# Performance work log

Hardware: AMD Instinct MI355X
Metric: run time of the kernel (lower is better)

Reference implementation:

```python
import jax, jax.numpy as jnp
import numpy as np

N = 100000
E = 1600000
DIN = 165
DH = 128


def setup_inputs() -> dict:
    key = jax.random.key(0)
    ks = jax.random.split(key, 10)
    def nrm(k, shape, scale=0.1):
        return jax.random.normal(k, shape, dtype=jnp.float32) * scale
    x = jax.random.normal(ks[0], (N, DIN), dtype=jnp.float32)
    edge_index = jax.random.randint(ks[1], (2, E), 0, N, dtype=jnp.int64)
    return dict(
        x=x,
        edge_index=edge_index,
        fb_w1=nrm(ks[2], (DIN, DIN // 2)),
        fb_w2=nrm(ks[3], (DIN // 2, DIN)),
        sage_wl=nrm(ks[4], (DIN, DH)),
        sage_bl=jnp.zeros((DH,), jnp.float32),
        sage_wr=nrm(ks[5], (DIN, DH)),
        gat_w=nrm(ks[6], (DH, DH // 2)),
        gat_att_src=nrm(ks[7], (DH // 2,)),
        gat_att_dst=nrm(ks[8], (DH // 2,)),
        gat_b=jnp.zeros((DH // 2,), jnp.float32),
        cheb_w=nrm(ks[9], (DH // 2, 1)),
        cheb_b=jnp.zeros((1,), jnp.float32),
    )


def _segment_softmax(logits, seg, num_segments):
    mx = jax.ops.segment_max(logits, seg, num_segments=num_segments)
    e = jnp.exp(logits - mx[seg])
    s = jax.ops.segment_sum(e, seg, num_segments=num_segments)
    return e / (s[seg] + 1e-16)


def reference(x, edge_index, fb_w1, fb_w2, sage_wl, sage_bl, sage_wr,
              gat_w, gat_att_src, gat_att_dst, gat_b, cheb_w, cheb_b):
    n = x.shape[0]
    src, dst = edge_index[0], edge_index[1]

    # FeatureBooster: scatter over batch=arange(n) is identity for max and sum,
    # so max_result == sum_result == x and y = sigmoid(mlp(x) + mlp(x)).
    m = jnp.maximum(x @ fb_w1, 0.0) @ fb_w2
    x = x * jax.nn.sigmoid(m + m)

    # SAGEConv (mean aggregation): out = lin_l(mean_agg(x_src -> dst)) + lin_r(x)
    agg = jax.ops.segment_sum(x[src], dst, num_segments=n)  # [n, DIN]
    cnt = jax.ops.segment_sum(jnp.ones((src.shape[0],), x.dtype), dst, num_segments=n)
    agg = agg / jnp.maximum(cnt, 1.0)[:, None]
    x = agg @ sage_wl + sage_bl + x @ sage_wr
    x = jnp.maximum(x, 0.0)  # relu; dropout is identity in eval mode

    # GATConv (heads=1) with default add_self_loops=True
    ar = jnp.arange(n, dtype=src.dtype)
    si = jnp.concatenate([src, ar])
    di = jnp.concatenate([dst, ar])
    h = x @ gat_w                      # [n, 64]
    a_s = h @ gat_att_src              # [n]
    a_d = h @ gat_att_dst              # [n]
    e = a_s[si] + a_d[di]
    e = jnp.where(e > 0, e, 0.2 * e)   # leaky_relu slope 0.2
    alpha = _segment_softmax(e, di, n)
    x = jax.ops.segment_sum(h[si] * alpha[:, None], di, num_segments=n) + gat_b
    x = jnp.maximum(x, 0.0)

    # ChebConv with K=1: T_0(x) = x, so it's a plain linear layer.
    x = x @ cheb_w + cheb_b
    return jax.nn.sigmoid(x)
```

## Files before the change

### kernel.cpp

```cpp
#include <hip/hip_runtime.h>
#include <hip/hip_bf16.h>

#define N_NODES 100000
#define N_EDGES 1600000
#define DIN 165
#define DHID 82
#define DH 128
#define DG 64

typedef _Float16 f16;
typedef f16 f16x8 __attribute__((ext_vector_type(8)));
typedef f16 f16x4 __attribute__((ext_vector_type(4)));
typedef f16 f16x2 __attribute__((ext_vector_type(2)));
typedef float f32x4 __attribute__((ext_vector_type(4)));

#define MFMA16(a, b, c) __builtin_amdgcn_mfma_f32_16x16x32_f16(a, b, c, 0, 0, 0)


__global__ __launch_bounds__(256) void xpad_kernel(const float* __restrict__ x,
                                                   f16* __restrict__ Xp) {
    int gid = blockIdx.x * 256 + threadIdx.x;
    int node = gid / 48, g = gid % 48;
    int col0 = g * 4;
    f16x4 o;
#pragma unroll
    for (int j = 0; j < 4; j++) {
        int c = col0 + j;
        o[j] = (f16)((c < DIN) ? x[(long)node * DIN + c] : 0.f);
    }
    *((f16x4*)(Xp + (long)node * 192 + col0)) = o;
}

__global__ __launch_bounds__(256) void h_kernel(const f16* __restrict__ Xp,
                                                const float* __restrict__ w1,
                                                f16* __restrict__ H) {
    int tid = threadIdx.x, wave = tid >> 6, lane = tid & 63;
    int q = lane >> 4, l16 = lane & 15;
    int blk = blockIdx.x;
    int g = (blk >> 3) & 1;
    int chunk = (blk & 7) + 8 * (blk >> 4);
    int nbase = g * 48;
    f16x8 bf[3][6];
#pragma unroll
    for (int nt = 0; nt < 3; nt++) {
        int col = nbase + nt * 16 + l16;
#pragma unroll
        for (int ks = 0; ks < 6; ks++) {
            int kb = ks * 32 + q * 8;
            f16x8 b;
#pragma unroll
            for (int j = 0; j < 8; j++) {
                int k = kb + j;
                b[j] = (f16)((k < DIN && col < DHID) ? w1[k * DHID + col] : 0.f);
            }
            bf[nt][ks] = b;
        }
    }
    for (int mt = chunk * 4 + wave; mt < 6250; mt += 768) {
        const f16* xr = Xp + (long)(mt * 16 + l16) * 192;
        f32x4 acc[3];
#pragma unroll
        for (int nt = 0; nt < 3; nt++) acc[nt] = (f32x4){0.f, 0.f, 0.f, 0.f};
#pragma unroll
        for (int ks = 0; ks < 6; ks++) {
            f16x8 a = *((const f16x8*)(xr + ks * 32 + q * 8));
#pragma unroll
            for (int nt = 0; nt < 3; nt++) acc[nt] = MFMA16(a, bf[nt][ks], acc[nt]);
        }
#pragma unroll
        for (int nt = 0; nt < 3; nt++) {
            int col = nbase + nt * 16 + l16;
#pragma unroll
            for (int r = 0; r < 4; r++) {
                int node = mt * 16 + q * 4 + r;
                H[(long)node * 96 + col] = (f16)fmaxf(acc[nt][r], 0.f);
            }
        }
    }
}

__global__ __launch_bounds__(256) void y_kernel(const f16* __restrict__ Xp,
                                                const f16* __restrict__ H,
                                                const float* __restrict__ w2,
                                                f16* __restrict__ Y) {
    int tid = threadIdx.x, wave = tid >> 6, lane = tid & 63;
    int q = lane >> 4, l16 = lane & 15;
    int blk = blockIdx.x;
    int g = (blk >> 3) & 3;
    int chunk = (blk & 7) + 8 * (blk >> 5);
    int nbase = g * 48;
    f16x8 bf[3][3];
#pragma unroll
    for (int nt = 0; nt < 3; nt++) {
        int col = nbase + nt * 16 + l16;
#pragma unroll
        for (int ks = 0; ks < 3; ks++) {
            int kb = ks * 32 + q * 8;
            f16x8 b;
#pragma unroll
            for (int j = 0; j < 8; j++) {
                int k = kb + j;
                b[j] = (f16)((k < DHID && col < DIN) ? w2[k * DIN + col] : 0.f);
            }
            bf[nt][ks] = b;
        }
    }
    for (int mt = chunk * 4 + wave; mt < 6250; mt += 768) {
        const f16* hr = H + (long)(mt * 16 + l16) * 96;
        f32x4 acc[3];
#pragma unroll
        for (int nt = 0; nt < 3; nt++) acc[nt] = (f32x4){0.f, 0.f, 0.f, 0.f};
#pragma unroll
        for (int ks = 0; ks < 3; ks++) {
            f16x8 a = *((const f16x8*)(hr + ks * 32 + q * 8));
#pragma unroll
            for (int nt = 0; nt < 3; nt++) acc[nt] = MFMA16(a, bf[nt][ks], acc[nt]);
        }
#pragma unroll
        for (int nt = 0; nt < 3; nt++) {
            int col = nbase + nt * 16 + l16;
#pragma unroll
            for (int r = 0; r < 4; r++) {
                int node = mt * 16 + q * 4 + r;
                float gg = 1.f / (1.f + __expf(-2.f * acc[nt][r]));
                float xv = (float)Xp[(long)node * 192 + col];
                Y[(long)node * 192 + col] = (f16)(xv * gg);
            }
        }
    }
}

__global__ __launch_bounds__(256) void sage_lin_kernel(const f16* __restrict__ Y,
                                                       const float* __restrict__ wl,
                                                       const float* __restrict__ wr,
                                                       const float* __restrict__ bl,
                                                       f16* __restrict__ t_l,
                                                       f16* __restrict__ x2) {
    int tid = threadIdx.x, wave = tid >> 6, lane = tid & 63;
    int q = lane >> 4, l16 = lane & 15;
    int blk = blockIdx.x;
    int g = (blk >> 3) & 3;
    int chunk = (blk & 7) + 8 * (blk >> 5);
    bool isR = (g >= 2);
    const float* W = isR ? wr : wl;
    int cbase = (g & 1) * 64;
    f16x8 bf[4][6];
    float blv[4];
#pragma unroll
    for (int nt = 0; nt < 4; nt++) {
        int col = cbase + nt * 16 + l16;
        blv[nt] = isR ? bl[col] : 0.f;
#pragma unroll
        for (int ks = 0; ks < 6; ks++) {
            int kb = ks * 32 + q * 8;
            f16x8 b;
#pragma unroll
            for (int j = 0; j < 8; j++) {
                int k = kb + j;
                b[j] = (f16)((k < DIN) ? W[k * DH + col] : 0.f);
            }
            bf[nt][ks] = b;
        }
    }
    for (int mt = chunk * 4 + wave; mt < 6250; mt += 768) {
        const f16* yrow = Y + (long)(mt * 16 + l16) * 192;
        f32x4 acc[4];
#pragma unroll
        for (int nt = 0; nt < 4; nt++) acc[nt] = (f32x4){0.f, 0.f, 0.f, 0.f};
#pragma unroll
        for (int ks = 0; ks < 6; ks++) {
            f16x8 a = *((const f16x8*)(yrow + ks * 32 + q * 8));
#pragma unroll
            for (int nt = 0; nt < 4; nt++) acc[nt] = MFMA16(a, bf[nt][ks], acc[nt]);
        }
#pragma unroll
        for (int nt = 0; nt < 4; nt++) {
            int col = cbase + nt * 16 + l16;
#pragma unroll
            for (int r = 0; r < 4; r++) {
                int node = mt * 16 + q * 4 + r;
                if (isR)
                    x2[(long)node * DH + col] = (f16)(acc[nt][r] + blv[nt]);
                else
                    t_l[(long)node * DH + col] = (f16)acc[nt][r];
            }
        }
    }
}

__global__ __launch_bounds__(256) void rank_kernel(const int* __restrict__ dst,
                                                   int* __restrict__ cnt,
                                                   int* __restrict__ rank) {
    int e = blockIdx.x * 256 + threadIdx.x;
    rank[e] = atomicAdd(&cnt[dst[e]], 1);
}

__global__ __launch_bounds__(1024) void scan1_kernel(const int* __restrict__ cnt,
                                                     int* __restrict__ rowptr,
                                                     int* __restrict__ bsum) {
    __shared__ int wsum[16];
    int tid = threadIdx.x, lane = tid & 63, wid = tid >> 6;
    int i = blockIdx.x * 1024 + tid;
    int v = (i < N_NODES) ? cnt[i] : 0;
    int xv = v;
#pragma unroll
    for (int off = 1; off < 64; off <<= 1) {
        int t = __shfl_up(xv, off);
        if (lane >= off) xv += t;
    }
    if (lane == 63) wsum[wid] = xv;
    __syncthreads();
    if (wid == 0 && lane < 16) {
        int wv = wsum[lane];
#pragma unroll
        for (int off = 1; off < 16; off <<= 1) {
            int t = __shfl_up(wv, off);
            if (lane >= off) wv += t;
        }
        wsum[lane] = wv;
    }
    __syncthreads();
    int off0 = wid ? wsum[wid - 1] : 0;
    if (i < N_NODES) rowptr[i] = off0 + xv - v;
    if (tid == 1023) bsum[blockIdx.x] = off0 + xv;
}

__global__ __launch_bounds__(64) void scan2_kernel(const int* __restrict__ bsum,
                                                   int* __restrict__ boff,
                                                   int* __restrict__ rowptr,
                                                   int nblocks) {
    int lane = threadIdx.x;
    int c = 0;
    for (int base = 0; base < nblocks; base += 64) {
        int idx = base + lane;
        int v = (idx < nblocks) ? bsum[idx] : 0;
        int xv = v;
#pragma unroll
        for (int off = 1; off < 64; off <<= 1) {
            int t = __shfl_up(xv, off);
            if (lane >= off) xv += t;
        }
        if (idx < nblocks) boff[idx] = c + xv - v;
        c += __shfl(xv, 63);
    }
    if (lane == 0) rowptr[N_NODES] = c;
}

__global__ __launch_bounds__(1024) void scan3_kernel(int* __restrict__ rowptr,
                                                     const int* __restrict__ boff) {
    int i = blockIdx.x * 1024 + threadIdx.x;
    if (i < N_NODES) rowptr[i] += boff[blockIdx.x];
}

__global__ __launch_bounds__(256) void fill_kernel(const int* __restrict__ src,
                                                   const int* __restrict__ dst,
                                                   const int* __restrict__ rank,
                                                   const int* __restrict__ rowptr,
                                                   int* __restrict__ esrc) {
    int e = blockIdx.x * 256 + threadIdx.x;
    int d = dst[e];
    int pos = rowptr[d] + rank[e];
    __builtin_nontemporal_store(src[e], &esrc[pos]);
}

__global__ __launch_bounds__(256) void sage_agg_kernel(const f16* __restrict__ t_l,
                                                       const int* __restrict__ rowptr,
                                                       const int* __restrict__ esrc,
                                                       f16* __restrict__ x2) {
    int wid = threadIdx.x >> 6, lane = threadIdx.x & 63;
    int i = blockIdx.x * 4 + wid;
    int r0 = rowptr[i], r1 = rowptr[i + 1];
    int quarter = lane >> 4, fq = lane & 15;
    float acc[8];
#pragma unroll
    for (int k = 0; k < 8; k++) acc[k] = 0.f;
    for (int e0 = r0; e0 < r1; e0 += 64) {
        int cnt = min(64, r1 - e0);
        int sn_v = (lane < cnt) ? esrc[e0 + lane] : 0;
        int jmax = (cnt + 3) >> 2;
        for (int j = 0; j < jmax; j++) {
            int idx = 4 * j + quarter;
            int sn = __shfl(sn_v, idx);
            float v = (idx < cnt) ? 1.f : 0.f;
            f16x8 p = *((const f16x8*)(t_l + ((long)sn << 7) + fq * 8));
#pragma unroll
            for (int k = 0; k < 8; k++) acc[k] = fmaf(v, (float)p[k], acc[k]);
        }
    }
#pragma unroll
    for (int k = 0; k < 8; k++) {
        acc[k] += __shfl_xor(acc[k], 16);
        acc[k] += __shfl_xor(acc[k], 32);
    }
    if (quarter == 0) {
        float inv = 1.f / fmaxf((float)(r1 - r0), 1.f);
        f16x8* xp = (f16x8*)(x2 + (long)i * DH + fq * 8);
        f16x8 pre = *xp;
        f16x8 o;
#pragma unroll
        for (int k = 0; k < 8; k++) o[k] = (f16)fmaxf((float)pre[k] + acc[k] * inv, 0.f);
        *xp = o;
    }
}

__global__ __launch_bounds__(256) void gat_h_kernel(const f16* __restrict__ x2,
                                                    const float* __restrict__ gw,
                                                    const float* __restrict__ att_s_w,
                                                    const float* __restrict__ att_d_w,
                                                    f16* __restrict__ h,
                                                    float* __restrict__ a_s,
                                                    float* __restrict__ a_d) {
    int tid = threadIdx.x, wave = tid >> 6, lane = tid & 63;
    int q = lane >> 4, l16 = lane & 15;
    f16x8 bf[4][4];
    float asw[4], adw[4];
#pragma unroll
    for (int nt = 0; nt < 4; nt++) {
        int col = nt * 16 + l16;
        asw[nt] = att_s_w[col];
        adw[nt] = att_d_w[col];
#pragma unroll
        for (int ks = 0; ks < 4; ks++) {
            int kb = ks * 32 + q * 8;
            f16x8 b;
#pragma unroll
            for (int j = 0; j < 8; j++) b[j] = (f16)gw[(kb + j) * DG + col];
            bf[nt][ks] = b;
        }
    }
    int stride = gridDim.x * 4;
    for (int mt = blockIdx.x * 4 + wave; mt < 6250; mt += stride) {
        const f16* xr = x2 + (long)(mt * 16 + l16) * DH;
        f32x4 acc[4];
#pragma unroll
        for (int nt = 0; nt < 4; nt++) acc[nt] = (f32x4){0.f, 0.f, 0.f, 0.f};
#pragma unroll
        for (int ks = 0; ks < 4; ks++) {
            f16x8 a = *((const f16x8*)(xr + ks * 32 + q * 8));
#pragma unroll
            for (int nt = 0; nt < 4; nt++) acc[nt] = MFMA16(a, bf[nt][ks], acc[nt]);
        }
#pragma unroll
        for (int r = 0; r < 4; r++) {
            int node = mt * 16 + q * 4 + r;
            float vs = 0.f, vd = 0.f;
#pragma unroll
            for (int nt = 0; nt < 4; nt++) {
                float hv = acc[nt][r];
                h[(long)node * DG + nt * 16 + l16] = (f16)hv;
                vs += hv * asw[nt];
                vd += hv * adw[nt];
            }
#pragma unroll
            for (int off = 1; off < 16; off <<= 1) {
                vs += __shfl_xor(vs, off);
                vd += __shfl_xor(vd, off);
            }
            if (l16 == 0) {
                a_s[node] = vs;
                a_d[node] = vd;
            }
        }
    }
}

__device__ __forceinline__ float leaky02(float v) { return v > 0.f ? v : 0.2f * v; }

__global__ __launch_bounds__(256) void gat_agg_kernel(const f16* __restrict__ h,
                                                      const float* __restrict__ a_s,
                                                      const float* __restrict__ a_d,
                                                      const int* __restrict__ rowptr,
                                                      const int* __restrict__ esrc,
                                                      const float* __restrict__ gat_b,
                                                      const float* __restrict__ cheb_w,
                                                      const float* __restrict__ cheb_b,
                                                      float* __restrict__ out) {
    int wid = threadIdx.x >> 6, lane = threadIdx.x & 63;
    int i = blockIdx.x * 4 + wid;
    int r0 = rowptr[i], r1 = rowptr[i + 1];
    int half = lane >> 5, fl = lane & 31;
    float adi = a_d[i];
    float accx = 0.f, accy = 0.f, sv = 0.f;
    for (int e0 = r0; e0 < r1; e0 += 64) {
        int cnt = min(64, r1 - e0);
        int sn_v = (lane < cnt) ? esrc[e0 + lane] : 0;
        float ev = 0.f;
        if (lane < cnt) ev = __expf(leaky02(a_s[sn_v] + adi));
        sv += ev;
        int jmax = (cnt + 1) >> 1;
        for (int j = 0; j < jmax; j++) {
            int idx = 2 * j + half;
            int sn = __shfl(sn_v, idx);
            float w = __shfl(ev, idx);
            f16x2 p = *((const f16x2*)(h + ((long)sn << 6) + 2 * fl));
            accx = fmaf(w, (float)p.x, accx);
            accy = fmaf(w, (float)p.y, accy);
        }
    }
#pragma unroll
    for (int off = 32; off > 0; off >>= 1) sv += __shfl_xor(sv, off);
    accx += __shfl_xor(accx, 32);
    accy += __shfl_xor(accy, 32);
    float wself = __expf(leaky02(a_s[i] + adi));
    float s = sv + wself;
    f16x2 ph = *((const f16x2*)(h + ((long)i << 6) + 2 * fl));
    accx = fmaf(wself, (float)ph.x, accx);
    accy = fmaf(wself, (float)ph.y, accy);
    float inv = 1.f / s;
    float ox = fmaxf(accx * inv + gat_b[2 * fl], 0.f);
    float oy = fmaxf(accy * inv + gat_b[2 * fl + 1], 0.f);
    float z = ox * cheb_w[2 * fl] + oy * cheb_w[2 * fl + 1];
#pragma unroll
    for (int off = 16; off > 0; off >>= 1) z += __shfl_xor(z, off);
    if (lane == 0) out[i] = 1.f / (1.f + __expf(-(z + cheb_b[0])));
}

extern "C" void kernel_launch(void* const* d_in, const int* in_sizes, int n_in,
                              void* d_out, int out_size, void* d_ws, size_t ws_size,
                              hipStream_t stream) {
    const float* x       = (const float*)d_in[0];
    const int*   eidx    = (const int*)d_in[1];
    const float* fb_w1   = (const float*)d_in[2];
    const float* fb_w2   = (const float*)d_in[3];
    const float* sage_wl = (const float*)d_in[4];
    const float* sage_bl = (const float*)d_in[5];
    const float* sage_wr = (const float*)d_in[6];
    const float* gat_w   = (const float*)d_in[7];
    const float* att_src = (const float*)d_in[8];
    const float* att_dst = (const float*)d_in[9];
    const float* gat_b   = (const float*)d_in[10];
    const float* cheb_w  = (const float*)d_in[11];
    const float* cheb_b  = (const float*)d_in[12];

    const int* src = eidx;
    const int* dst = eidx + N_EDGES;

    char* base = (char*)d_ws;
    f16* Xp = (f16*)base;
    f16* H  = (f16*)(base + 38400000);
    f16* Y  = (f16*)(base + 57600000);
    f16* t_l = (f16*)base;
    f16* x2  = (f16*)(base + 25600000);
    f16* h   = Y;
    float* a_s = (float*)(base + 70400000);
    float* a_d = a_s + N_NODES;
    int* rowptr = (int*)(base + 96000000);
    int* cnt  = rowptr + (N_NODES + 1);
    int* esrc = cnt + N_NODES;
    int* rank = esrc + N_EDGES;
    int* bsum = rank + N_EDGES;
    int* boff = bsum + 128;

    const int SCAN_BLOCKS = (N_NODES + 1023) / 1024;

    hipMemsetAsync(cnt, 0, N_NODES * sizeof(int), stream);

    rank_kernel<<<N_EDGES / 256, 256, 0, stream>>>(dst, cnt, rank);
    scan1_kernel<<<SCAN_BLOCKS, 1024, 0, stream>>>(cnt, rowptr, bsum);
    scan2_kernel<<<1, 64, 0, stream>>>(bsum, boff, rowptr, SCAN_BLOCKS);
    scan3_kernel<<<SCAN_BLOCKS, 1024, 0, stream>>>(rowptr, boff);
    fill_kernel<<<N_EDGES / 256, 256, 0, stream>>>(src, dst, rank, rowptr, esrc);
    xpad_kernel<<<(N_NODES * 48) / 256, 256, 0, stream>>>(x, Xp);
    h_kernel<<<384, 256, 0, stream>>>(Xp, fb_w1, H);
    y_kernel<<<768, 256, 0, stream>>>(Xp, H, fb_w2, Y);
    sage_lin_kernel<<<768, 256, 0, stream>>>(Y, sage_wl, sage_wr, sage_bl, t_l, x2);
    sage_agg_kernel<<<N_NODES / 4, 256, 0, stream>>>(t_l, rowptr, esrc, x2);
    gat_h_kernel<<<392, 256, 0, stream>>>(x2, gat_w, att_src, att_dst, h, a_s, a_d);
    gat_agg_kernel<<<N_NODES / 4, 256, 0, stream>>>(h, a_s, a_d, rowptr, esrc, gat_b,
                                                    cheb_w, cheb_b, (float*)d_out);
}
```

Measured before the change: 502.7 us.

## Fuse CSR build into xpad and h kernels; widen GAT gather to f16x4

Merges the edge rank atomic pass into the x padding kernel and the CSR fill pass into the first feature-booster GEMM kernel, which removes two launches and lets the index work overlap with dense work. The fill loop now runs as a grid-stride loop over 384 blocks before the MFMA work, so it lengthens that kernel. The GAT aggregation switches from two half-waves with f16x2 loads to four quarter-waves with f16x4 loads, processing four edges per iteration. The epilogue is restricted to one quarter with vectorised bias and weight loads.

```diff
diff --git a/kernel.cpp b/kernel.cpp
--- a/kernel.cpp
+++ b/kernel.cpp
@@ -17,9 +17,13 @@
 #define MFMA16(a, b, c) __builtin_amdgcn_mfma_f32_16x16x32_f16(a, b, c, 0, 0, 0)
 
 
-__global__ __launch_bounds__(256) void xpad_kernel(const float* __restrict__ x,
-                                                   f16* __restrict__ Xp) {
+__global__ __launch_bounds__(256) void rank_xpad_kernel(const float* __restrict__ x,
+                                                        f16* __restrict__ Xp,
+                                                        const int* __restrict__ dst,
+                                                        int* __restrict__ cnt,
+                                                        int* __restrict__ rank) {
     int gid = blockIdx.x * 256 + threadIdx.x;
+    if (gid < N_EDGES) rank[gid] = atomicAdd(&cnt[dst[gid]], 1);
     int node = gid / 48, g = gid % 48;
     int col0 = g * 4;
     f16x4 o;
@@ -31,10 +35,79 @@
     *((f16x4*)(Xp + (long)node * 192 + col0)) = o;
 }
 
-__global__ __launch_bounds__(256) void h_kernel(const f16* __restrict__ Xp,
-                                                const float* __restrict__ w1,
-                                                f16* __restrict__ H) {
+__global__ __launch_bounds__(1024) void scan1_kernel(const int* __restrict__ cnt,
+                                                     int* __restrict__ rowptr,
+                                                     int* __restrict__ bsum) {
+    __shared__ int wsum[16];
+    int tid = threadIdx.x, lane = tid & 63, wid = tid >> 6;
+    int i = blockIdx.x * 1024 + tid;
+    int v = (i < N_NODES) ? cnt[i] : 0;
+    int xv = v;
+#pragma unroll
+    for (int off = 1; off < 64; off <<= 1) {
+        int t = __shfl_up(xv, off);
+        if (lane >= off) xv += t;
+    }
+    if (lane == 63) wsum[wid] = xv;
+    __syncthreads();
+    if (wid == 0 && lane < 16) {
+        int wv = wsum[lane];
+#pragma unroll
+        for (int off = 1; off < 16; off <<= 1) {
+            int t = __shfl_up(wv, off);
+            if (lane >= off) wv += t;
+        }
+        wsum[lane] = wv;
+    }
+    __syncthreads();
+    int off0 = wid ? wsum[wid - 1] : 0;
+    if (i < N_NODES) rowptr[i] = off0 + xv - v;
+    if (tid == 1023) bsum[blockIdx.x] = off0 + xv;
+}
+
+__global__ __launch_bounds__(64) void scan2_kernel(const int* __restrict__ bsum,
+                                                   int* __restrict__ boff,
+                                                   int* __restrict__ rowptr,
+                                                   int nblocks) {
+    int lane = threadIdx.x;
+    int c = 0;
+    for (int base = 0; base < nblocks; base += 64) {
+        int idx = base + lane;
+        int v = (idx < nblocks) ? bsum[idx] : 0;
+        int xv = v;
+#pragma unroll
+        for (int off = 1; off < 64; off <<= 1) {
+            int t = __shfl_up(xv, off);
+            if (lane >= off) xv += t;
+        }
+        if (idx < nblocks) boff[idx] = c + xv - v;
+        c += __shfl(xv, 63);
+    }
+    if (lane == 0) rowptr[N_NODES] = c;
+}
+
+__global__ __launch_bounds__(1024) void scan3_kernel(int* __restrict__ rowptr,
+                                                     const int* __restrict__ boff) {
+    int i = blockIdx.x * 1024 + threadIdx.x;
+    if (i < N_NODES) rowptr[i] += boff[blockIdx.x];
+}
+
+__global__ __launch_bounds__(256) void h_fill_kernel(const f16* __restrict__ Xp,
+                                                     const float* __restrict__ w1,
+                                                     f16* __restrict__ H,
+                                                     const int* __restrict__ src,
+                                                     const int* __restrict__ dst,
+                                                     const int* __restrict__ rank,
+                                                     const int* __restrict__ rowptr,
+                                                     int* __restrict__ esrc) {
     int tid = threadIdx.x, wave = tid >> 6, lane = tid & 63;
+    {
+        int tg = blockIdx.x * 256 + tid;
+        for (int e = tg; e < N_EDGES; e += 384 * 256) {
+            int d = dst[e];
+            __builtin_nontemporal_store(src[e], &esrc[rowptr[d] + rank[e]]);
+        }
+    }
     int q = lane >> 4, l16 = lane & 15;
     int blk = blockIdx.x;
     int g = (blk >> 3) & 1;
@@ -188,81 +261,6 @@
     }
 }
 
-__global__ __launch_bounds__(256) void rank_kernel(const int* __restrict__ dst,
-                                                   int* __restrict__ cnt,
-                                                   int* __restrict__ rank) {
-    int e = blockIdx.x * 256 + threadIdx.x;
-    rank[e] = atomicAdd(&cnt[dst[e]], 1);
-}
-
-__global__ __launch_bounds__(1024) void scan1_kernel(const int* __restrict__ cnt,
-                                                     int* __restrict__ rowptr,
-                                                     int* __restrict__ bsum) {
-    __shared__ int wsum[16];
-    int tid = threadIdx.x, lane = tid & 63, wid = tid >> 6;
-    int i = blockIdx.x * 1024 + tid;
-    int v = (i < N_NODES) ? cnt[i] : 0;
-    int xv = v;
-#pragma unroll
-    for (int off = 1; off < 64; off <<= 1) {
-        int t = __shfl_up(xv, off);
-        if (lane >= off) xv += t;
-    }
-    if (lane == 63) wsum[wid] = xv;
-    __syncthreads();
-    if (wid == 0 && lane < 16) {
-        int wv = wsum[lane];
-#pragma unroll
-        for (int off = 1; off < 16; off <<= 1) {
-            int t = __shfl_up(wv, off);
-            if (lane >= off) wv += t;
-        }
-        wsum[lane] = wv;
-    }
-    __syncthreads();
-    int off0 = wid ? wsum[wid - 1] : 0;
-    if (i < N_NODES) rowptr[i] = off0 + xv - v;
-    if (tid == 1023) bsum[blockIdx.x] = off0 + xv;
-}
-
-__global__ __launch_bounds__(64) void scan2_kernel(const int* __restrict__ bsum,
-                                                   int* __restrict__ boff,
-                                                   int* __restrict__ rowptr,
-                                                   int nblocks) {
-    int lane = threadIdx.x;
-    int c = 0;
-    for (int base = 0; base < nblocks; base += 64) {
-        int idx = base + lane;
-        int v = (idx < nblocks) ? bsum[idx] : 0;
-        int xv = v;
-#pragma unroll
-        for (int off = 1; off < 64; off <<= 1) {
-            int t = __shfl_up(xv, off);
-            if (lane >= off) xv += t;
-        }
-        if (idx < nblocks) boff[idx] = c + xv - v;
-        c += __shfl(xv, 63);
-    }
-    if (lane == 0) rowptr[N_NODES] = c;
-}
-
-__global__ __launch_bounds__(1024) void scan3_kernel(int* __restrict__ rowptr,
-                                                     const int* __restrict__ boff) {
-    int i = blockIdx.x * 1024 + threadIdx.x;
-    if (i < N_NODES) rowptr[i] += boff[blockIdx.x];
-}
-
-__global__ __launch_bounds__(256) void fill_kernel(const int* __restrict__ src,
-                                                   const int* __restrict__ dst,
-                                                   const int* __restrict__ rank,
-                                                   const int* __restrict__ rowptr,
-                                                   int* __restrict__ esrc) {
-    int e = blockIdx.x * 256 + threadIdx.x;
-    int d = dst[e];
-    int pos = rowptr[d] + rank[e];
-    __builtin_nontemporal_store(src[e], &esrc[pos]);
-}
-
 __global__ __launch_bounds__(256) void sage_agg_kernel(const f16* __restrict__ t_l,
                                                        const int* __restrict__ rowptr,
                                                        const int* __restrict__ esrc,
@@ -378,41 +376,52 @@
     int wid = threadIdx.x >> 6, lane = threadIdx.x & 63;
     int i = blockIdx.x * 4 + wid;
     int r0 = rowptr[i], r1 = rowptr[i + 1];
-    int half = lane >> 5, fl = lane & 31;
+    int quarter = lane >> 4, fq = lane & 15;
     float adi = a_d[i];
-    float accx = 0.f, accy = 0.f, sv = 0.f;
+    float acc[4] = {0.f, 0.f, 0.f, 0.f};
+    float sv = 0.f;
     for (int e0 = r0; e0 < r1; e0 += 64) {
         int cnt = min(64, r1 - e0);
         int sn_v = (lane < cnt) ? esrc[e0 + lane] : 0;
         float ev = 0.f;
         if (lane < cnt) ev = __expf(leaky02(a_s[sn_v] + adi));
         sv += ev;
-        int jmax = (cnt + 1) >> 1;
+        int jmax = (cnt + 3) >> 2;
         for (int j = 0; j < jmax; j++) {
-            int idx = 2 * j + half;
+            int idx = 4 * j + quarter;
             int sn = __shfl(sn_v, idx);
             float w = __shfl(ev, idx);
-            f16x2 p = *((const f16x2*)(h + ((long)sn << 6) + 2 * fl));
-            accx = fmaf(w, (float)p.x, accx);
-            accy = fmaf(w, (float)p.y, accy);
+            f16x4 p = *((const f16x4*)(h + ((long)sn << 6) + fq * 4));
+#pragma unroll
+            for (int k = 0; k < 4; k++) acc[k] = fmaf(w, (float)p[k], acc[k]);
         }
     }
 #pragma unroll
     for (int off = 32; off > 0; off >>= 1) sv += __shfl_xor(sv, off);
-    accx += __shfl_xor(accx, 32);
-    accy += __shfl_xor(accy, 32);
-    float wself = __expf(leaky02(a_s[i] + adi));
-    float s = sv + wself;
-    f16x2 ph = *((const f16x2*)(h + ((long)i << 6) + 2 * fl));
-    accx = fmaf(wself, (float)ph.x, accx);
-    accy = fmaf(wself, (float)ph.y, accy);
-    float inv = 1.f / s;
-    float ox = fmaxf(accx * inv + gat_b[2 * fl], 0.f);
-    float oy = fmaxf(accy * inv + gat_b[2 * fl + 1], 0.f);
-    float z = ox * cheb_w[2 * fl] + oy * cheb_w[2 * fl + 1];
-#pragma unroll
-    for (int off = 16; off > 0; off >>= 1) z += __shfl_xor(z, off);
-    if (lane == 0) out[i] = 1.f / (1.f + __expf(-(z + cheb_b[0])));
+#pragma unroll
+    for (int k = 0; k < 4; k++) {
+        acc[k] += __shfl_xor(acc[k], 16);
+        acc[k] += __shfl_xor(acc[k], 32);
+    }
+    if (quarter == 0) {
+        float wself = __expf(leaky02(a_s[i] + adi));
+        float s = sv + wself;
+        f16x4 ph = *((const f16x4*)(h + ((long)i << 6) + fq * 4));
+        float4 gb = ((const float4*)gat_b)[fq];
+        float4 cw = ((const float4*)cheb_w)[fq];
+        float gbv[4] = {gb.x, gb.y, gb.z, gb.w};
+        float cwv[4] = {cw.x, cw.y, cw.z, cw.w};
+        float inv = 1.f / s;
+        float z = 0.f;
+#pragma unroll
+        for (int k = 0; k < 4; k++) {
+            float o = fmaxf(fmaf(wself, (float)ph[k], acc[k]) * inv + gbv[k], 0.f);
+            z = fmaf(o, cwv[k], z);
+        }
+#pragma unroll
+        for (int off = 8; off > 0; off >>= 1) z += __shfl_xor(z, off);
+        if (fq == 0) out[i] = 1.f / (1.f + __expf(-(z + cheb_b[0])));
+    }
 }
 
 extern "C" void kernel_launch(void* const* d_in, const int* in_sizes, int n_in,
@@ -455,13 +464,11 @@
 
     hipMemsetAsync(cnt, 0, N_NODES * sizeof(int), stream);
 
-    rank_kernel<<<N_EDGES / 256, 256, 0, stream>>>(dst, cnt, rank);
+    rank_xpad_kernel<<<(N_NODES * 48) / 256, 256, 0, stream>>>(x, Xp, dst, cnt, rank);
     scan1_kernel<<<SCAN_BLOCKS, 1024, 0, stream>>>(cnt, rowptr, bsum);
     scan2_kernel<<<1, 64, 0, stream>>>(bsum, boff, rowptr, SCAN_BLOCKS);
     scan3_kernel<<<SCAN_BLOCKS, 1024, 0, stream>>>(rowptr, boff);
-    fill_kernel<<<N_EDGES / 256, 256, 0, stream>>>(src, dst, rank, rowptr, esrc);
-    xpad_kernel<<<(N_NODES * 48) / 256, 256, 0, stream>>>(x, Xp);
-    h_kernel<<<384, 256, 0, stream>>>(Xp, fb_w1, H);
+    h_fill_kernel<<<384, 256, 0, stream>>>(Xp, fb_w1, H, src, dst, rank, rowptr, esrc);
     y_kernel<<<768, 256, 0, stream>>>(Xp, H, fb_w2, Y);
     sage_lin_kernel<<<768, 256, 0, stream>>>(Y, sage_wl, sage_wr, sage_bl, t_l, x2);
     sage_agg_kernel<<<N_NODES / 4, 256, 0, stream>>>(t_l, rowptr, esrc, x2);
```

Measured after the change: 484.5 us. 3.6% less time.
